# Optimization experiments

Hardware: AMD Instinct MI355X
Metric: run time of the kernel (lower is better)

Reference implementation:

```python
import jax, jax.numpy as jnp
import numpy as np

B, H, S, DK, DV = 2, 16, 2048, 128, 128


def setup_inputs() -> dict:
    key = jax.random.key(0)
    kq, kk, kv = jax.random.split(key, 3)
    query = jax.random.normal(kq, (B, H, S, DK), dtype=jnp.float32)
    k_ = jax.random.normal(kk, (B, H, S, DK), dtype=jnp.float32)
    value = jax.random.normal(kv, (B, H, S, DV), dtype=jnp.float32)
    # causal mask: True = masked out (upper triangle above diagonal)
    causal = ~jnp.tril(jnp.ones((S, S), dtype=bool))
    mask = jnp.broadcast_to(causal[None, None, :, :], (B, 1, S, S))
    return {"query": query, "key": k_, "value": value, "mask": mask}


def reference(query, key, value, mask):
    d_k = query.shape[-1]
    # scores: (B, H, Sq, Sk)
    scores = jnp.einsum("bhqd,bhkd->bhqk", query, key) / jnp.sqrt(jnp.float32(d_k))
    scores = jnp.where(mask, -jnp.inf, scores)
    attention_weights = jax.nn.softmax(scores, axis=-1)
    # dropout p=0.0 (eval) -> identity
    output = jnp.einsum("bhqk,bhkv->bhqv", attention_weights, value)
    return (output, attention_weights)
```

## Files before the change

kernel.cpp:

```cpp
#include <hip/hip_runtime.h>
#include <hip/hip_bf16.h>


typedef __attribute__((ext_vector_type(4))) float  f32x4;
typedef __attribute__((ext_vector_type(8))) short  short8;
typedef __attribute__((ext_vector_type(4))) short  short4v;

#define S_LEN 2048
#define DKK   128
#define QBLK  64
#define KBLK  64
#define NBH   32

__device__ __forceinline__ short f2bf(float f) {
    unsigned u = __builtin_bit_cast(unsigned, f);
    u += 0x7FFF + ((u >> 16) & 1);
    return (short)(u >> 16);
}

__device__ __forceinline__ void g2l16(const void* g, void* l) {
    __builtin_amdgcn_global_load_lds(
        (const __attribute__((address_space(1))) unsigned int*)g,
        (__attribute__((address_space(3))) unsigned int*)l, 16, 0, 0);
}


__global__ __launch_bounds__(256) void conv_k(const float* __restrict__ K,
                                              short* __restrict__ Kb) {
    const int NCH = NBH * S_LEN * (DKK / 8);
    for (int g = blockIdx.x * 256 + threadIdx.x; g < NCH; g += gridDim.x * 256) {
        const int row = g >> 4;
        const int c   = g & 15;
        const float* p = K + (size_t)row * DKK + c * 8;
        f32x4 a = *(const f32x4*)p;
        f32x4 b = *(const f32x4*)(p + 4);
        short8 r;
        #pragma unroll
        for (int j = 0; j < 4; ++j) {
            r[j]     = f2bf(a[j]);
            r[4 + j] = f2bf(b[j]);
        }
        *(short8*)(Kb + (size_t)row * DKK + (size_t)(c ^ (row & 7)) * 8) = r;
    }
}

__global__ __launch_bounds__(256) void conv_vt(const float* __restrict__ V,
                                               short* __restrict__ VT) {
    __shared__ short tile[64][130];
    const int bh = blockIdx.x >> 5;
    const int kt = blockIdx.x & 31;
    const float* Vb = V + ((size_t)bh * S_LEN + kt * 64) * DKK;
    const int t  = threadIdx.x;
    const int k8 = t >> 5, d0 = (t & 31) * 4;
    #pragma unroll
    for (int it = 0; it < 8; ++it) {
        int k = it * 8 + k8;
        f32x4 v = *(const f32x4*)(Vb + (size_t)k * DKK + d0);
        #pragma unroll
        for (int j = 0; j < 4; ++j) tile[k][d0 + j] = f2bf(v[j]);
    }
    __syncthreads();
    const int d = t >> 1, half = t & 1;
    short* outb = VT + (size_t)bh * DKK * S_LEN + (size_t)d * S_LEN + kt * 64;
    #pragma unroll
    for (int cc = 0; cc < 4; ++cc) {
        short8 r;
        #pragma unroll
        for (int j = 0; j < 8; ++j) r[j] = tile[half * 32 + cc * 8 + j][d];
        int cp = (half * 4 + cc) ^ (d & 7);
        *(short8*)(outb + cp * 8) = r;
    }
}


__global__ __launch_bounds__(256) void attn_main(
    const float* __restrict__ Qf, const short* __restrict__ Kb,
    const short* __restrict__ VT, float* __restrict__ O,
    float* __restrict__ W)
{
    __shared__ __align__(16) short kT[2][KBLK * DKK];
    __shared__ __align__(16) short vtT[2][DKK * KBLK];
    __shared__ __align__(16) short pT[4][16 * KBLK];

    const int tid  = threadIdx.x;
    const int lane = tid & 63;
    const int w    = tid >> 6;
    const int lg   = lane >> 4;
    const int lr   = lane & 15;
    const int s7   = lr & 7;

    const int bh = (blockIdx.x & 7) * 4 + ((blockIdx.x >> 3) & 3);
    const int qt = 31 - (blockIdx.x >> 5);
    const int q0 = qt * QBLK;
    const int qbase = q0 + w * 16;
    const int kend = q0 + QBLK;
    const int ntk  = qt + 1;
    const int qg   = qbase + lr;

    const short* Kbh = Kb + (size_t)bh * S_LEN * DKK;
    const short* VTb = VT + (size_t)bh * DKK * S_LEN;
    float* Ob = O + (size_t)bh * S_LEN * DKK;
    float* Wb = W + (size_t)bh * S_LEN * S_LEN;

    const float QSCALE = 0.08838834764831845f * 1.4426950408889634f;
    short8 qf[4];
    {
        const float* qp = Qf + ((size_t)bh * S_LEN + qg) * DKK + lg * 8;
        #pragma unroll
        for (int ds = 0; ds < 4; ++ds) {
            f32x4 a = *(const f32x4*)(qp + ds * 32);
            f32x4 b = *(const f32x4*)(qp + ds * 32 + 4);
            short8 r;
            #pragma unroll
            for (int j = 0; j < 4; ++j) {
                r[j]     = f2bf(a[j] * QSCALE);
                r[4 + j] = f2bf(b[j] * QSCALE);
            }
            qf[ds] = r;
        }
    }

    auto stage_k = [&](int buf, int kt_) {
        const char* gk = (const char*)(Kbh + (size_t)kt_ * KBLK * DKK);
        char* lk = (char*)kT[buf];
        #pragma unroll
        for (int i = 0; i < 4; ++i)
            g2l16(gk + i * 4096 + tid * 16, lk + i * 4096 + w * 1024);
    };
    auto stage_v = [&](int buf, int kt_) {
        const char* gv = (const char*)VTb + (size_t)kt_ * KBLK * 2;
        char* lv = (char*)vtT[buf];
        #pragma unroll
        for (int i = 0; i < 4; ++i) {
            int L = i * 4096 + tid * 16;
            g2l16(gv + (size_t)(L >> 7) * 4096 + (L & 127),
                  lv + i * 4096 + w * 1024);
        }
    };

    stage_k(0, 0);
    stage_v(0, 0);

    float lsum = 0.f;
    {
        const char* kG = (const char*)Kbh;
        for (int kt_ = 0; kt_ < ntk; ++kt_) {
            const int k0 = kt_ * KBLK;
            #pragma unroll
            for (int t = 0; t < 4; ++t) {
                const char* rowp = kG + (size_t)(k0 + 16 * t + lr) * 256;
                f32x4 d = {0.f, 0.f, 0.f, 0.f};
                __builtin_amdgcn_s_setprio(1);
                #pragma unroll
                for (int ds = 0; ds < 4; ++ds)
                    d = __builtin_amdgcn_mfma_f32_16x16x32_bf16(
                            *(const short8*)(rowp + (((lg + ds * 4) ^ s7) * 16)),
                            qf[ds], d, 0, 0, 0);
                __builtin_amdgcn_s_setprio(0);
                const int kb = k0 + 16 * t + lg * 4;
                #pragma unroll
                for (int r = 0; r < 4; ++r)
                    lsum += (kb + r <= qg) ? exp2f(d[r]) : 0.f;
            }
        }
    }
    lsum += __shfl_xor(lsum, 16);
    lsum += __shfl_xor(lsum, 32);
    const float invl = 1.0f / lsum;

    f32x4 acc[8];
    #pragma unroll
    for (int i = 0; i < 8; ++i) acc[i] = (f32x4){0.f, 0.f, 0.f, 0.f};

    int cur = 0;
    for (int kt_ = 0; kt_ < ntk; ++kt_) {
        __syncthreads();
        if (kt_ + 1 < ntk) { stage_k(cur ^ 1, kt_ + 1); stage_v(cur ^ 1, kt_ + 1); }
        const int k0 = kt_ * KBLK;
        const char* kBc = (const char*)kT[cur];
        const char* vBc = (const char*)vtT[cur];
        char* pBc = (char*)pT[w];

        #pragma unroll
        for (int t = 0; t < 4; ++t) {
            const int krow = t * 16 + lr;
            f32x4 d = {0.f, 0.f, 0.f, 0.f};
            __builtin_amdgcn_s_setprio(1);
            #pragma unroll
            for (int ds = 0; ds < 4; ++ds) {
                const int off = (krow * 256 + ds * 64 + lg * 16) ^ (s7 << 4);
                d = __builtin_amdgcn_mfma_f32_16x16x32_bf16(
                        *(const short8*)(kBc + off), qf[ds], d, 0, 0, 0);
            }
            __builtin_amdgcn_s_setprio(0);
            const int kb = k0 + 16 * t + lg * 4;
            f32x4 pv;
            short4v pb;
            #pragma unroll
            for (int r = 0; r < 4; ++r) {
                const float p = (kb + r <= qg) ? exp2f(d[r]) * invl : 0.f;
                pv[r] = p;
                pb[r] = f2bf(p);
            }
            *(f32x4*)(Wb + (size_t)qg * S_LEN + kb) = pv;
            const int poff = lr * 128 + (((16 * t + lg * 4) * 2) ^ (s7 << 4));
            *(short4v*)(pBc + poff) = pb;
        }
        #pragma unroll
        for (int h = 0; h < 2; ++h) {
            const int poff = lr * 128 + ((h * 64 + lg * 16) ^ (s7 << 4));
            short8 pa = *(const short8*)(pBc + poff);
            __builtin_amdgcn_s_setprio(1);
            #pragma unroll
            for (int nt = 0; nt < 8; ++nt) {
                const int voff = (nt * 16 + lr) * 128 + ((h * 64 + lg * 16) ^ (s7 << 4));
                short8 vf = *(const short8*)(vBc + voff);
                acc[nt] = __builtin_amdgcn_mfma_f32_16x16x32_bf16(pa, vf, acc[nt], 0, 0, 0);
            }
            __builtin_amdgcn_s_setprio(0);
        }
        cur ^= 1;
    }

    #pragma unroll
    for (int nt = 0; nt < 8; ++nt)
        #pragma unroll
        for (int r = 0; r < 4; ++r)
            Ob[(size_t)(qbase + lg * 4 + r) * DKK + nt * 16 + lr] = acc[nt][r];

    const int zc = S_LEN - kend;
    if (zc > 0) {
        const int yo = tid >> 2;
        const int xo = tid & 3;
        float* wrow = Wb + (size_t)(q0 + yo) * S_LEN + kend;
        const f32x4 z = {0.f, 0.f, 0.f, 0.f};
        for (int c = xo * 4; c < zc; c += 16)
            *(f32x4*)(wrow + c) = z;
    }
}

extern "C" void kernel_launch(void* const* d_in, const int* in_sizes, int n_in,
                              void* d_out, int out_size, void* d_ws, size_t ws_size,
                              hipStream_t stream) {
    const float* Q = (const float*)d_in[0];
    const float* K = (const float*)d_in[1];
    const float* V = (const float*)d_in[2];
    float* O = (float*)d_out;
    float* W = (float*)d_out + (size_t)NBH * S_LEN * DKK;

    const size_t TEN = (size_t)NBH * S_LEN * DKK;
    short* Kb  = (short*)d_ws;
    short* VTw = Kb + TEN;

    conv_k <<<2048, 256, 0, stream>>>(K, Kb);
    conv_vt<<<1024, 256, 0, stream>>>(V, VTw);
    attn_main<<<1024, 256, 0, stream>>>(Q, Kb, VTw, O, W);
}
```

Measured before the change: 261.0 us.

## Halve key tile to 32 and skip fully masked per-wave tiles

Shrinks the key/value tile from 64 to 32 rows and adds a per-wave liveness check, so waves whose 16 query rows sit entirely before a key tile skip the MFMA work and just write zeros. The row-sum pass now stages K through LDS with double buffering instead of reading K directly from global memory. Block-to-(head, query tile) mapping alternates the query-tile order by batch to balance causal work across XCDs, and the V transpose swizzle changes to match the narrower tile. In exchange, the kernel runs twice as many loop iterations with more barriers and smaller copies per step.

```diff
diff --git a/kernel.cpp b/kernel.cpp
--- a/kernel.cpp
+++ b/kernel.cpp
@@ -9,7 +9,7 @@
 #define S_LEN 2048
 #define DKK   128
 #define QBLK  64
-#define KBLK  64
+#define KBLK  32
 #define NBH   32
 
 __device__ __forceinline__ short f2bf(float f) {
@@ -67,7 +67,7 @@
         short8 r;
         #pragma unroll
         for (int j = 0; j < 8; ++j) r[j] = tile[half * 32 + cc * 8 + j][d];
-        int cp = (half * 4 + cc) ^ (d & 7);
+        int cp = half * 4 + (cc ^ (d & 3));
         *(short8*)(outb + cp * 8) = r;
     }
 }
@@ -80,7 +80,7 @@
 {
     __shared__ __align__(16) short kT[2][KBLK * DKK];
     __shared__ __align__(16) short vtT[2][DKK * KBLK];
-    __shared__ __align__(16) short pT[4][16 * KBLK];
+    __shared__ __align__(16) short pT[4][16 * 64];
 
     const int tid  = threadIdx.x;
     const int lane = tid & 63;
@@ -89,13 +89,18 @@
     const int lr   = lane & 15;
     const int s7   = lr & 7;
 
-    const int bh = (blockIdx.x & 7) * 4 + ((blockIdx.x >> 3) & 3);
-    const int qt = 31 - (blockIdx.x >> 5);
-    const int q0 = qt * QBLK;
+    const int i     = blockIdx.x;
+    const int xcd   = i & 7;
+    const int j     = (i >> 3) & 31;
+    const int batch = i >> 8;
+    const int bh    = xcd * 4 + batch;
+    const int qt    = (batch & 1) ? j : (31 - j);
+
+    const int q0    = qt * QBLK;
     const int qbase = q0 + w * 16;
-    const int kend = q0 + QBLK;
-    const int ntk  = qt + 1;
-    const int qg   = qbase + lr;
+    const int kend  = q0 + QBLK;
+    const int ntk   = (qt + 1) * 2;
+    const int qg    = qbase + lr;
 
     const short* Kbh = Kb + (size_t)bh * S_LEN * DKK;
     const short* VTb = VT + (size_t)bh * DKK * S_LEN;
@@ -112,50 +117,54 @@
             f32x4 b = *(const f32x4*)(qp + ds * 32 + 4);
             short8 r;
             #pragma unroll
-            for (int j = 0; j < 4; ++j) {
-                r[j]     = f2bf(a[j] * QSCALE);
-                r[4 + j] = f2bf(b[j] * QSCALE);
+            for (int jj = 0; jj < 4; ++jj) {
+                r[jj]     = f2bf(a[jj] * QSCALE);
+                r[4 + jj] = f2bf(b[jj] * QSCALE);
             }
             qf[ds] = r;
         }
     }
 
-    auto stage_k = [&](int buf, int kt_) {
-        const char* gk = (const char*)(Kbh + (size_t)kt_ * KBLK * DKK);
+    auto stage_k = [&](int buf, int kt32) {
+        const char* gk = (const char*)Kbh + (size_t)kt32 * (KBLK * DKK * 2);
         char* lk = (char*)kT[buf];
         #pragma unroll
-        for (int i = 0; i < 4; ++i)
-            g2l16(gk + i * 4096 + tid * 16, lk + i * 4096 + w * 1024);
+        for (int ii = 0; ii < 2; ++ii)
+            g2l16(gk + ii * 4096 + tid * 16, lk + ii * 4096 + w * 1024);
     };
-    auto stage_v = [&](int buf, int kt_) {
-        const char* gv = (const char*)VTb + (size_t)kt_ * KBLK * 2;
+    auto stage_v = [&](int buf, int kt32) {
+        const char* gv = (const char*)VTb + (size_t)kt32 * 64;
         char* lv = (char*)vtT[buf];
         #pragma unroll
-        for (int i = 0; i < 4; ++i) {
-            int L = i * 4096 + tid * 16;
-            g2l16(gv + (size_t)(L >> 7) * 4096 + (L & 127),
-                  lv + i * 4096 + w * 1024);
+        for (int ii = 0; ii < 2; ++ii) {
+            const int L = ii * 4096 + tid * 16;
+            g2l16(gv + (size_t)(L >> 6) * (S_LEN * 2) + (L & 63),
+                  lv + ii * 4096 + w * 1024);
         }
     };
 
+    auto k_frag = [&](const char* kBc, int t, int ds) -> short8 {
+        const int off = ((16 * t + lr) * 256 + (ds * 64 + lg * 16)) ^ (s7 << 4);
+        return *(const short8*)(kBc + off);
+    };
+
+    float lsum = 0.f;
+    int cur = 0;
     stage_k(0, 0);
-    stage_v(0, 0);
-
-    float lsum = 0.f;
-    {
-        const char* kG = (const char*)Kbh;
-        for (int kt_ = 0; kt_ < ntk; ++kt_) {
-            const int k0 = kt_ * KBLK;
-            #pragma unroll
-            for (int t = 0; t < 4; ++t) {
-                const char* rowp = kG + (size_t)(k0 + 16 * t + lr) * 256;
+    for (int kt_ = 0; kt_ < ntk; ++kt_) {
+        __syncthreads();
+        if (kt_ + 1 < ntk) stage_k(cur ^ 1, kt_ + 1);
+        const int k0 = kt_ * KBLK;
+        if (k0 <= qbase + 15) {
+            const char* kBc = (const char*)kT[cur];
+            #pragma unroll
+            for (int t = 0; t < 2; ++t) {
                 f32x4 d = {0.f, 0.f, 0.f, 0.f};
                 __builtin_amdgcn_s_setprio(1);
                 #pragma unroll
                 for (int ds = 0; ds < 4; ++ds)
                     d = __builtin_amdgcn_mfma_f32_16x16x32_bf16(
-                            *(const short8*)(rowp + (((lg + ds * 4) ^ s7) * 16)),
-                            qf[ds], d, 0, 0, 0);
+                            k_frag(kBc, t, ds), qf[ds], d, 0, 0, 0);
                 __builtin_amdgcn_s_setprio(0);
                 const int kb = k0 + 16 * t + lg * 4;
                 #pragma unroll
@@ -163,6 +172,7 @@
                     lsum += (kb + r <= qg) ? exp2f(d[r]) : 0.f;
             }
         }
+        cur ^= 1;
     }
     lsum += __shfl_xor(lsum, 16);
     lsum += __shfl_xor(lsum, 32);
@@ -170,54 +180,59 @@
 
     f32x4 acc[8];
     #pragma unroll
-    for (int i = 0; i < 8; ++i) acc[i] = (f32x4){0.f, 0.f, 0.f, 0.f};
-
-    int cur = 0;
+    for (int ii = 0; ii < 8; ++ii) acc[ii] = (f32x4){0.f, 0.f, 0.f, 0.f};
+
+    __syncthreads();
+    cur = 0;
+    stage_k(0, 0);
+    stage_v(0, 0);
     for (int kt_ = 0; kt_ < ntk; ++kt_) {
         __syncthreads();
         if (kt_ + 1 < ntk) { stage_k(cur ^ 1, kt_ + 1); stage_v(cur ^ 1, kt_ + 1); }
         const int k0 = kt_ * KBLK;
-        const char* kBc = (const char*)kT[cur];
-        const char* vBc = (const char*)vtT[cur];
-        char* pBc = (char*)pT[w];
-
-        #pragma unroll
-        for (int t = 0; t < 4; ++t) {
-            const int krow = t * 16 + lr;
-            f32x4 d = {0.f, 0.f, 0.f, 0.f};
-            __builtin_amdgcn_s_setprio(1);
-            #pragma unroll
-            for (int ds = 0; ds < 4; ++ds) {
-                const int off = (krow * 256 + ds * 64 + lg * 16) ^ (s7 << 4);
-                d = __builtin_amdgcn_mfma_f32_16x16x32_bf16(
-                        *(const short8*)(kBc + off), qf[ds], d, 0, 0, 0);
-            }
-            __builtin_amdgcn_s_setprio(0);
-            const int kb = k0 + 16 * t + lg * 4;
-            f32x4 pv;
-            short4v pb;
-            #pragma unroll
-            for (int r = 0; r < 4; ++r) {
-                const float p = (kb + r <= qg) ? exp2f(d[r]) * invl : 0.f;
-                pv[r] = p;
-                pb[r] = f2bf(p);
-            }
-            *(f32x4*)(Wb + (size_t)qg * S_LEN + kb) = pv;
-            const int poff = lr * 128 + (((16 * t + lg * 4) * 2) ^ (s7 << 4));
-            *(short4v*)(pBc + poff) = pb;
-        }
-        #pragma unroll
-        for (int h = 0; h < 2; ++h) {
-            const int poff = lr * 128 + ((h * 64 + lg * 16) ^ (s7 << 4));
+        const bool live = (k0 <= qbase + 15);
+        if (live) {
+            const char* kBc = (const char*)kT[cur];
+            const char* vBc = (const char*)vtT[cur];
+            char* pBc = (char*)pT[w];
+            #pragma unroll
+            for (int t = 0; t < 2; ++t) {
+                f32x4 d = {0.f, 0.f, 0.f, 0.f};
+                __builtin_amdgcn_s_setprio(1);
+                #pragma unroll
+                for (int ds = 0; ds < 4; ++ds)
+                    d = __builtin_amdgcn_mfma_f32_16x16x32_bf16(
+                            k_frag(kBc, t, ds), qf[ds], d, 0, 0, 0);
+                __builtin_amdgcn_s_setprio(0);
+                const int kb = k0 + 16 * t + lg * 4;
+                f32x4 pv;
+                short4v pb;
+                #pragma unroll
+                for (int r = 0; r < 4; ++r) {
+                    const float p = (kb + r <= qg) ? exp2f(d[r]) * invl : 0.f;
+                    pv[r] = p;
+                    pb[r] = f2bf(p);
+                }
+                *(f32x4*)(Wb + (size_t)qg * S_LEN + kb) = pv;
+                const int poff = lr * 128 + ((((16 * t + lg * 4) * 2)) ^ (s7 << 4));
+                *(short4v*)(pBc + poff) = pb;
+            }
+            const int poff = lr * 128 + ((lg * 16) ^ (s7 << 4));
             short8 pa = *(const short8*)(pBc + poff);
             __builtin_amdgcn_s_setprio(1);
             #pragma unroll
             for (int nt = 0; nt < 8; ++nt) {
-                const int voff = (nt * 16 + lr) * 128 + ((h * 64 + lg * 16) ^ (s7 << 4));
+                const int dv   = nt * 16 + lr;
+                const int voff = dv * 64 + ((lg * 16) ^ ((dv & 3) << 4));
                 short8 vf = *(const short8*)(vBc + voff);
                 acc[nt] = __builtin_amdgcn_mfma_f32_16x16x32_bf16(pa, vf, acc[nt], 0, 0, 0);
             }
             __builtin_amdgcn_s_setprio(0);
+        } else {
+            const f32x4 z = {0.f, 0.f, 0.f, 0.f};
+            #pragma unroll
+            for (int t = 0; t < 2; ++t)
+                *(f32x4*)(Wb + (size_t)qg * S_LEN + k0 + 16 * t + lg * 4) = z;
         }
         cur ^= 1;
     }
```

Result: slower. 281.4 us (+7.8%).

## Stage K through LDS in sum pass, prefetch V, use fast exp2 and nontemporal stores

Applied to the files above, without the earlier changes.

The row-sum pass now double-buffers K tiles into LDS instead of reading K fragments straight from global memory, and the first V tiles are prefetched during that pass. The main pass re-stages K from tile 0. Raw exp2 replaces exp2f, the bf16 conversion uses the library intrinsic, and the large attention-weight and zero-fill writes use nontemporal stores to reduce cache pollution. This adds barriers to the first pass and reloads K twice through LDS, and the buffer reuse across the two passes needs care to stay correct.

```diff
diff --git a/kernel.cpp b/kernel.cpp
--- a/kernel.cpp
+++ b/kernel.cpp
@@ -13,9 +13,7 @@
 #define NBH   32
 
 __device__ __forceinline__ short f2bf(float f) {
-    unsigned u = __builtin_bit_cast(unsigned, f);
-    u += 0x7FFF + ((u >> 16) & 1);
-    return (short)(u >> 16);
+    return __builtin_bit_cast(short, __float2bfloat16(f));
 }
 
 __device__ __forceinline__ void g2l16(const void* g, void* l) {
@@ -93,9 +91,9 @@
     const int qt = 31 - (blockIdx.x >> 5);
     const int q0 = qt * QBLK;
     const int qbase = q0 + w * 16;
-    const int kend = q0 + QBLK;
-    const int ntk  = qt + 1;
-    const int qg   = qbase + lr;
+    const int kend  = q0 + QBLK;
+    const int ntk   = qt + 1;
+    const int qg    = qbase + lr;
 
     const short* Kbh = Kb + (size_t)bh * S_LEN * DKK;
     const short* VTb = VT + (size_t)bh * DKK * S_LEN;
@@ -112,9 +110,9 @@
             f32x4 b = *(const f32x4*)(qp + ds * 32 + 4);
             short8 r;
             #pragma unroll
-            for (int j = 0; j < 4; ++j) {
-                r[j]     = f2bf(a[j] * QSCALE);
-                r[4 + j] = f2bf(b[j] * QSCALE);
+            for (int jj = 0; jj < 4; ++jj) {
+                r[jj]     = f2bf(a[jj] * QSCALE);
+                r[4 + jj] = f2bf(b[jj] * QSCALE);
             }
             qf[ds] = r;
         }
@@ -128,41 +126,47 @@
             g2l16(gk + i * 4096 + tid * 16, lk + i * 4096 + w * 1024);
     };
     auto stage_v = [&](int buf, int kt_) {
-        const char* gv = (const char*)VTb + (size_t)kt_ * KBLK * 2;
+        const char* gv = (const char*)VTb + (size_t)kt_ * (KBLK * 2);
         char* lv = (char*)vtT[buf];
         #pragma unroll
         for (int i = 0; i < 4; ++i) {
-            int L = i * 4096 + tid * 16;
-            g2l16(gv + (size_t)(L >> 7) * 4096 + (L & 127),
+            const int L = i * 4096 + tid * 16;
+            g2l16(gv + (size_t)(L >> 7) * (S_LEN * 2) + (L & 127),
                   lv + i * 4096 + w * 1024);
         }
+    };
+
+    auto k_frag = [&](const char* kBc, int t, int ds) -> short8 {
+        const int off = ((16 * t + lr) * 256 + ds * 64 + lg * 16) ^ (s7 << 4);
+        return *(const short8*)(kBc + off);
     };
 
     stage_k(0, 0);
     stage_v(0, 0);
+    if (ntk > 1) stage_v(1, 1);
 
     float lsum = 0.f;
-    {
-        const char* kG = (const char*)Kbh;
-        for (int kt_ = 0; kt_ < ntk; ++kt_) {
-            const int k0 = kt_ * KBLK;
-            #pragma unroll
-            for (int t = 0; t < 4; ++t) {
-                const char* rowp = kG + (size_t)(k0 + 16 * t + lr) * 256;
-                f32x4 d = {0.f, 0.f, 0.f, 0.f};
-                __builtin_amdgcn_s_setprio(1);
-                #pragma unroll
-                for (int ds = 0; ds < 4; ++ds)
-                    d = __builtin_amdgcn_mfma_f32_16x16x32_bf16(
-                            *(const short8*)(rowp + (((lg + ds * 4) ^ s7) * 16)),
-                            qf[ds], d, 0, 0, 0);
-                __builtin_amdgcn_s_setprio(0);
-                const int kb = k0 + 16 * t + lg * 4;
-                #pragma unroll
-                for (int r = 0; r < 4; ++r)
-                    lsum += (kb + r <= qg) ? exp2f(d[r]) : 0.f;
-            }
-        }
+    int cur = 0;
+    for (int kt_ = 0; kt_ < ntk; ++kt_) {
+        __syncthreads();
+        if (kt_ + 1 < ntk) stage_k(cur ^ 1, kt_ + 1);
+        const int k0 = kt_ * KBLK;
+        const char* kBc = (const char*)kT[cur];
+        #pragma unroll
+        for (int t = 0; t < 4; ++t) {
+            f32x4 d = {0.f, 0.f, 0.f, 0.f};
+            __builtin_amdgcn_s_setprio(1);
+            #pragma unroll
+            for (int ds = 0; ds < 4; ++ds)
+                d = __builtin_amdgcn_mfma_f32_16x16x32_bf16(
+                        k_frag(kBc, t, ds), qf[ds], d, 0, 0, 0);
+            __builtin_amdgcn_s_setprio(0);
+            const int kb = k0 + 16 * t + lg * 4;
+            #pragma unroll
+            for (int r = 0; r < 4; ++r)
+                lsum += (kb + r <= qg) ? __builtin_amdgcn_exp2f(d[r]) : 0.f;
+        }
+        cur ^= 1;
     }
     lsum += __shfl_xor(lsum, 16);
     lsum += __shfl_xor(lsum, 32);
@@ -170,12 +174,17 @@
 
     f32x4 acc[8];
     #pragma unroll
-    for (int i = 0; i < 8; ++i) acc[i] = (f32x4){0.f, 0.f, 0.f, 0.f};
-
-    int cur = 0;
+    for (int ii = 0; ii < 8; ++ii) acc[ii] = (f32x4){0.f, 0.f, 0.f, 0.f};
+
+    __syncthreads();
+    cur = 0;
+    stage_k(0, 0);
     for (int kt_ = 0; kt_ < ntk; ++kt_) {
         __syncthreads();
-        if (kt_ + 1 < ntk) { stage_k(cur ^ 1, kt_ + 1); stage_v(cur ^ 1, kt_ + 1); }
+        if (kt_ + 1 < ntk) {
+            stage_k(cur ^ 1, kt_ + 1);
+            if (kt_ >= 1) stage_v(cur ^ 1, kt_ + 1);
+        }
         const int k0 = kt_ * KBLK;
         const char* kBc = (const char*)kT[cur];
         const char* vBc = (const char*)vtT[cur];
@@ -183,26 +192,23 @@
 
         #pragma unroll
         for (int t = 0; t < 4; ++t) {
-            const int krow = t * 16 + lr;
             f32x4 d = {0.f, 0.f, 0.f, 0.f};
             __builtin_amdgcn_s_setprio(1);
             #pragma unroll
-            for (int ds = 0; ds < 4; ++ds) {
-                const int off = (krow * 256 + ds * 64 + lg * 16) ^ (s7 << 4);
+            for (int ds = 0; ds < 4; ++ds)
                 d = __builtin_amdgcn_mfma_f32_16x16x32_bf16(
-                        *(const short8*)(kBc + off), qf[ds], d, 0, 0, 0);
-            }
+                        k_frag(kBc, t, ds), qf[ds], d, 0, 0, 0);
             __builtin_amdgcn_s_setprio(0);
             const int kb = k0 + 16 * t + lg * 4;
             f32x4 pv;
             short4v pb;
             #pragma unroll
             for (int r = 0; r < 4; ++r) {
-                const float p = (kb + r <= qg) ? exp2f(d[r]) * invl : 0.f;
+                const float p = (kb + r <= qg) ? __builtin_amdgcn_exp2f(d[r]) * invl : 0.f;
                 pv[r] = p;
                 pb[r] = f2bf(p);
             }
-            *(f32x4*)(Wb + (size_t)qg * S_LEN + kb) = pv;
+            __builtin_nontemporal_store(pv, (f32x4*)(Wb + (size_t)qg * S_LEN + kb));
             const int poff = lr * 128 + (((16 * t + lg * 4) * 2) ^ (s7 << 4));
             *(short4v*)(pBc + poff) = pb;
         }
@@ -235,7 +241,7 @@
         float* wrow = Wb + (size_t)(q0 + yo) * S_LEN + kend;
         const f32x4 z = {0.f, 0.f, 0.f, 0.f};
         for (int c = xo * 4; c < zc; c += 16)
-            *(f32x4*)(wrow + c) = z;
+            __builtin_nontemporal_store(z, (f32x4*)(wrow + c));
     }
 }
 
```

Result: slower. 295.1 us (+13.1%).
